# Kernel optimization log

Measured on AMD Instinct MI355X. Metric: run time of the kernel, lower is better.

Reference implementation:

```python
import jax, jax.numpy as jnp
import numpy as np

B, S, D, H, HD = 1, 4096, 1024, 16, 64
BLOCK = 128   # Fixed1/Fixed2 block_size (paper default for EnWik8)
C = 32        # Fixed2 'c' parameter
NEG = -1e10   # large negative bias for masked positions (flax make_attention_mask)


def build_sparse_mask(n: int) -> jnp.ndarray:
    """Merged Fixed1 + Fixed2 causal mask, shape [1,1,n,n] bool."""
    r = jnp.arange(n)
    q = r[:, None]
    k = r[None, :]
    lower = k <= q
    fixed1 = (q // BLOCK) == (k // BLOCK)
    rem = k % BLOCK
    fixed2 = (rem == 0) | (rem >= BLOCK - C)
    mask = lower & (fixed1 | fixed2)
    return mask[None, None, :, :]


def setup_inputs() -> dict:
    key = jax.random.key(0)
    ks = jax.random.split(key, 5)
    sc = 1.0 / np.sqrt(D)
    return {
        "x": jax.random.normal(ks[0], (B, S, D), jnp.float32),
        "Wq": jax.random.normal(ks[1], (D, H, HD), jnp.float32) * sc,
        "bq": jnp.zeros((H, HD), jnp.float32),
        "Wk": jax.random.normal(ks[2], (D, H, HD), jnp.float32) * sc,
        "bk": jnp.zeros((H, HD), jnp.float32),
        "Wv": jax.random.normal(ks[3], (D, H, HD), jnp.float32) * sc,
        "bv": jnp.zeros((H, HD), jnp.float32),
        "Wo": jax.random.normal(ks[4], (H, HD, D), jnp.float32) * (1.0 / np.sqrt(H * HD)),
        "bo": jnp.zeros((D,), jnp.float32),
    }


def reference(x, Wq, bq, Wk, bk, Wv, bv, Wo, bo):
    # QKV projections: [B,S,D] -> [B,S,H,HD]
    q = jnp.einsum("bsd,dhk->bshk", x, Wq) + bq
    k = jnp.einsum("bsd,dhk->bshk", x, Wk) + bk
    v = jnp.einsum("bsd,dhk->bshk", x, Wv) + bv

    bias = jnp.where(build_sparse_mask(S), 0.0, NEG).astype(x.dtype)

    # flax dot_product_attention: scale query, scores + bias, softmax, weighted sum
    q = q / jnp.sqrt(jnp.asarray(HD, x.dtype))
    scores = jnp.einsum("bqhd,bkhd->bhqk", q, k) + bias
    probs = jax.nn.softmax(scores, axis=-1)
    ctx = jnp.einsum("bhqk,bkhd->bqhd", probs, v)

    # output projection over (h, d) axes
    return jnp.einsum("bqhd,hdf->bqf", ctx, Wo) + bo
```

## Files before the change

### kernel.cpp

```cpp
#include <hip/hip_runtime.h>
#include <stdint.h>


#define S_LEN 4096
#define DMODEL 1024

typedef __bf16 bf16x8 __attribute__((ext_vector_type(8)));
typedef float  f32x4  __attribute__((ext_vector_type(4)));

__device__ __forceinline__ uint16_t f2bf(float f) {
    uint32_t u = __builtin_bit_cast(uint32_t, f);
    u += 0x7fffu + ((u >> 16) & 1u);
    return (uint16_t)(u >> 16);
}

__device__ __forceinline__ uint32_t pack2bf(float lo, float hi) {
    return (uint32_t)f2bf(lo) | ((uint32_t)f2bf(hi) << 16);
}

__device__ __forceinline__ void gload_lds16(const uint16_t* g, uint16_t* l) {
    __builtin_amdgcn_global_load_lds(
        (const __attribute__((address_space(1))) void*)g,
        (__attribute__((address_space(3))) void*)l, 16, 0, 0);
}

__device__ __forceinline__ int key_of(int b, int ngc, int ch, int kl) {
    if (ch >= ngc) return b * 128 + (ch - ngc) * 64 + kl;
    int t = ch * 64 + kl;
    int kb = t / 33, rr = t - kb * 33;
    return kb * 128 + (rr == 0 ? 0 : 95 + rr);
}

__global__ __launch_bounds__(256) void cvt_x_kernel(const float* __restrict__ x,
                                                    uint16_t* __restrict__ xb) {
    int i = (blockIdx.x * 256 + threadIdx.x) * 4;
    const float4 v = *(const float4*)(x + i);
    ushort4 o;
    o.x = f2bf(v.x); o.y = f2bf(v.y); o.z = f2bf(v.z); o.w = f2bf(v.w);
    *(ushort4*)(xb + i) = o;
}

__global__ __launch_bounds__(256) void tpose4(const float* __restrict__ Wq,
                                              const float* __restrict__ Wk,
                                              const float* __restrict__ Wv,
                                              const float* __restrict__ Wo,
                                              uint16_t* __restrict__ wqkvt,
                                              uint16_t* __restrict__ wot) {
    __shared__ float tile[64][65];
    const int z = blockIdx.z;
    const float* src = (z == 0) ? Wq : (z == 1) ? Wk : (z == 2) ? Wv : Wo;
    uint16_t* dst = (z < 3) ? (wqkvt + (size_t)z * 1024 * 1024) : wot;
    const int ro = blockIdx.y * 64, co = blockIdx.x * 64;
    const int c = threadIdx.x & 63, r4 = threadIdx.x >> 6;
#pragma unroll
    for (int i = 0; i < 16; i++) {
        int r = i * 4 + r4;
        tile[r][c] = src[(size_t)(ro + r) * 1024 + co + c];
    }
    __syncthreads();
#pragma unroll
    for (int i = 0; i < 16; i++) {
        int cc = i * 4 + r4;
        dst[(size_t)(co + cc) * 1024 + ro + c] = f2bf(tile[c][cc]);
    }
}

template <int MODE>
__global__ __launch_bounds__(256) void gemm_bt(const uint16_t* __restrict__ A,
                                               const uint16_t* __restrict__ Bt,
                                               const float* __restrict__ bias0,
                                               const float* __restrict__ bias1,
                                               const float* __restrict__ bias2,
                                               uint16_t* __restrict__ Cb,
                                               float* __restrict__ Cf) {
    __shared__ __attribute__((aligned(16))) uint16_t As[128 * 64];
    __shared__ __attribute__((aligned(16))) uint16_t Bs[128 * 64];
    const int tid = threadIdx.x;
    const int wave = tid >> 6, lane = tid & 63;
    const int quad = lane >> 4, l16 = lane & 15;
    const int row0 = blockIdx.y * 128, col0 = blockIdx.x * 128;
    const int wm = (wave >> 1) * 64, wn = (wave & 1) * 64;
    const int srow = lane >> 3, scol = lane & 7;
    const int gcol = (scol ^ srow) * 8;
    const int sw = (l16 & 7);

    f32x4 acc[4][4];
    const f32x4 z4 = {0.f, 0.f, 0.f, 0.f};
#pragma unroll
    for (int i = 0; i < 4; i++)
#pragma unroll
        for (int j = 0; j < 4; j++) acc[i][j] = z4;

    for (int k0 = 0; k0 < 1024; k0 += 64) {
        __syncthreads();
#pragma unroll
        for (int i = 0; i < 4; i++) {
            int u = wave * 4 + i;
            int row = u * 8 + srow;
            gload_lds16(A  + (size_t)(row0 + row) * 1024 + k0 + gcol, As + u * 512);
            gload_lds16(Bt + (size_t)(col0 + row) * 1024 + k0 + gcol, Bs + u * 512);
        }
        __syncthreads();
#pragma unroll
        for (int kk = 0; kk < 2; kk++) {
            bf16x8 af[4], bfr[4];
#pragma unroll
            for (int mt = 0; mt < 4; mt++)
                af[mt] = *(const bf16x8*)(As + (wm + mt * 16 + l16) * 64 + ((kk * 4 + quad) ^ sw) * 8);
#pragma unroll
            for (int nt = 0; nt < 4; nt++)
                bfr[nt] = *(const bf16x8*)(Bs + (wn + nt * 16 + l16) * 64 + ((kk * 4 + quad) ^ sw) * 8);
#pragma unroll
            for (int mt = 0; mt < 4; mt++)
#pragma unroll
                for (int nt = 0; nt < 4; nt++) {
                    if (MODE == 0)
                        acc[mt][nt] = __builtin_amdgcn_mfma_f32_16x16x32_bf16(
                            bfr[nt], af[mt], acc[mt][nt], 0, 0, 0);
                    else
                        acc[mt][nt] = __builtin_amdgcn_mfma_f32_16x16x32_bf16(
                            af[mt], bfr[nt], acc[mt][nt], 0, 0, 0);
                }
        }
    }

    if (MODE == 0) {
#pragma unroll
        for (int nt = 0; nt < 4; nt++) {
            int n = col0 + wn + nt * 16 + quad * 4;
            int which = n >> 10, c = n & 1023;
            const float* bp = (which == 0) ? bias0 : (which == 1 ? bias1 : bias2);
            const float4 b4 = *(const float4*)(bp + c);
            float scv = (which == 0) ? 0.125f : 1.0f;
            uint16_t* op = Cb + (size_t)which * S_LEN * 1024 + c;
#pragma unroll
            for (int mt = 0; mt < 4; mt++) {
                int s = row0 + wm + mt * 16 + l16;
                ushort4 pkv;
                pkv.x = f2bf((acc[mt][nt][0] + b4.x) * scv);
                pkv.y = f2bf((acc[mt][nt][1] + b4.y) * scv);
                pkv.z = f2bf((acc[mt][nt][2] + b4.z) * scv);
                pkv.w = f2bf((acc[mt][nt][3] + b4.w) * scv);
                *(ushort4*)(op + (size_t)s * 1024) = pkv;
            }
        }
    } else {
#pragma unroll
        for (int nt = 0; nt < 4; nt++) {
            int n = col0 + wn + nt * 16 + l16;
            float bi = bias0[n];
#pragma unroll
            for (int mt = 0; mt < 4; mt++) {
                int row = row0 + wm + mt * 16 + quad * 4;
#pragma unroll
                for (int r = 0; r < 4; r++)
                    Cf[(size_t)(row + r) * 1024 + n] = acc[mt][nt][r] + bi;
            }
        }
    }
}

__global__ __launch_bounds__(512, 4) void attn_kernel(const uint16_t* __restrict__ Qg,
                                                      const uint16_t* __restrict__ Kg,
                                                      const uint16_t* __restrict__ Vg,
                                                      uint16_t* __restrict__ Og) {
    __shared__ __attribute__((aligned(16))) uint16_t SM[32768];
    uint16_t* Qs    = SM;
    uint16_t* Kbufs = SM + 8192;
    uint16_t* Vbufs = SM + 24576;

    const int h = blockIdx.y;
    const int b = (h < 8) ? (int)blockIdx.x : (31 - (int)blockIdx.x);
    const int tid = threadIdx.x;
    const int wave = tid >> 6, lane = tid & 63;
    const int quad = lane >> 4, l16 = lane & 15;
    const int grp = wave >> 2, wq = wave & 3;
    const int sw = (l16 & 7);

    const int nprev = 33 * b;
    const int ngc = (nprev + 63) >> 6;
    const int ntot = ngc + 2;
    const int nit = (ntot + 1) >> 1;
    const size_t hoff = (size_t)h * 64;

    const int kRow = wave * 8 + (lane >> 3);
    const int gCol = ((lane & 7) ^ (lane >> 3)) * 8;

#pragma unroll
    for (int i = 0; i < 2; i++) {
        int seg = i * 8 + wave;
        int row = seg * 8 + (lane >> 3);
        gload_lds16(Qg + (size_t)(b * 128 + row) * 1024 + hoff + gCol, Qs + seg * 512);
    }
#pragma unroll
    for (int g = 0; g < 2; g++) {
        if (g < ntot) {
            int key = key_of(b, ngc, g, kRow);
            gload_lds16(Kg + (size_t)key * 1024 + hoff + gCol,
                        Kbufs + g * 4096 + wave * 512);
        }
    }
    __syncthreads();

    float m_run[2], l_run[2];
    f32x4 o[4][2];
    const f32x4 z4 = {0.f, 0.f, 0.f, 0.f};
#pragma unroll
    for (int qt = 0; qt < 2; qt++) { m_run[qt] = -3e38f; l_run[qt] = 0.f; }
#pragma unroll
    for (int mt = 0; mt < 4; mt++) { o[mt][0] = z4; o[mt][1] = z4; }

    int cur = 0;
    for (int it = 0; it < nit; it++) {
        uint4 vreg[2];
#pragma unroll
        for (int g = 0; g < 2; g++) {
            int ch = 2 * it + g;
            if (ch < ntot) {
                int key = key_of(b, ngc, ch, lane);
                vreg[g] = *(const uint4*)(Vg + (size_t)key * 1024 + hoff + wave * 8);
            }
        }
#pragma unroll
        for (int g = 0; g < 2; g++) {
            int ch = 2 * (it + 1) + g;
            if (ch < ntot) {
                int key = key_of(b, ngc, ch, kRow);
                gload_lds16(Kg + (size_t)key * 1024 + hoff + gCol,
                            Kbufs + (cur ^ 1) * 8192 + g * 4096 + wave * 512);
            }
        }

        const int myc = 2 * it + grp;
        const bool have = (myc < ntot);
        uint32_t pk[4][2][2];
        float al[2] = {1.f, 1.f};
        if (have) {
            const uint16_t* Kc = Kbufs + cur * 8192 + grp * 4096;
            f32x4 s[4][2];
#pragma unroll
            for (int kt = 0; kt < 4; kt++) { s[kt][0] = z4; s[kt][1] = z4; }
#pragma unroll
            for (int kk = 0; kk < 2; kk++) {
                bf16x8 ka[4], qb[2];
#pragma unroll
                for (int kt = 0; kt < 4; kt++)
                    ka[kt] = *(const bf16x8*)(Kc + (kt * 16 + l16) * 64 + ((kk * 4 + quad) ^ sw) * 8);
#pragma unroll
                for (int qt = 0; qt < 2; qt++)
                    qb[qt] = *(const bf16x8*)(Qs + (wq * 32 + qt * 16 + l16) * 64 + ((kk * 4 + quad) ^ sw) * 8);
#pragma unroll
                for (int kt = 0; kt < 4; kt++)
#pragma unroll
                    for (int qt = 0; qt < 2; qt++)
                        s[kt][qt] = __builtin_amdgcn_mfma_f32_16x16x32_bf16(
                            ka[kt], qb[qt], s[kt][qt], 0, 0, 0);
            }
            if (myc >= ngc) {
                int cb = myc - ngc;
#pragma unroll
                for (int kt = 0; kt < 4; kt++) {
                    int keyl = cb * 64 + kt * 16 + quad * 4;
#pragma unroll
                    for (int qt = 0; qt < 2; qt++) {
                        int ql = wq * 32 + qt * 16 + l16;
#pragma unroll
                        for (int r = 0; r < 4; r++)
                            if (keyl + r > ql) s[kt][qt][r] = -1e30f;
                    }
                }
            } else if (myc == ngc - 1) {
#pragma unroll
                for (int kt = 0; kt < 4; kt++) {
                    int tg = myc * 64 + kt * 16 + quad * 4;
#pragma unroll
                    for (int r = 0; r < 4; r++)
                        if (tg + r >= nprev) {
                            s[kt][0][r] = -1e30f;
                            s[kt][1][r] = -1e30f;
                        }
                }
            }
#pragma unroll
            for (int qt = 0; qt < 2; qt++) {
                float mx = -3e38f;
#pragma unroll
                for (int kt = 0; kt < 4; kt++)
#pragma unroll
                    for (int r = 0; r < 4; r++) mx = fmaxf(mx, s[kt][qt][r]);
                mx = fmaxf(mx, __shfl_xor(mx, 16));
                mx = fmaxf(mx, __shfl_xor(mx, 32));
                float mn = fmaxf(m_run[qt], mx);
                float sub = fmaxf(mn, -1e20f);
                al[qt] = __expf(m_run[qt] - sub);
                m_run[qt] = mn;
                float ps = 0.f;
#pragma unroll
                for (int kt = 0; kt < 4; kt++) {
                    float p0 = __expf(s[kt][qt][0] - sub);
                    float p1 = __expf(s[kt][qt][1] - sub);
                    float p2 = __expf(s[kt][qt][2] - sub);
                    float p3 = __expf(s[kt][qt][3] - sub);
                    ps += (p0 + p1) + (p2 + p3);
                    pk[kt][qt][0] = pack2bf(p0, p1);
                    pk[kt][qt][1] = pack2bf(p2, p3);
                }
                ps += __shfl_xor(ps, 16);
                ps += __shfl_xor(ps, 32);
                l_run[qt] = l_run[qt] * al[qt] + ps;
            }
        }

#pragma unroll
        for (int g = 0; g < 2; g++) {
            int ch = 2 * it + g;
            if (ch < ntot) {
                uint16_t* Vd = Vbufs + g * 4096;
                uint32_t ww[4] = {vreg[g].x, vreg[g].y, vreg[g].z, vreg[g].w};
                const int kc = (lane >> 3), kin = (lane & 7);
#pragma unroll
                for (int j = 0; j < 4; j++) {
                    int hd0 = wave * 8 + 2 * j, hd1 = hd0 + 1;
                    Vd[hd0 * 64 + ((kc ^ (hd0 & 7)) * 8 + kin)] = (uint16_t)(ww[j] & 0xffffu);
                    Vd[hd1 * 64 + ((kc ^ (hd1 & 7)) * 8 + kin)] = (uint16_t)(ww[j] >> 16);
                }
            }
        }
        __syncthreads();

        if (have) {
            const uint16_t* Vc = Vbufs + grp * 4096;
#pragma unroll
            for (int mt = 0; mt < 4; mt++)
#pragma unroll
                for (int qt = 0; qt < 2; qt++)
#pragma unroll
                    for (int r = 0; r < 4; r++) o[mt][qt][r] *= al[qt];
            const int srcA = l16 + 32 * (quad & 1);
            const bool hi = (quad >> 1) != 0;
#pragma unroll
            for (int kk = 0; kk < 2; kk++) {
                bf16x8 va[4];
#pragma unroll
                for (int mt = 0; mt < 4; mt++)
                    va[mt] = *(const bf16x8*)(Vc + (mt * 16 + l16) * 64 + ((kk * 4 + quad) ^ sw) * 8);
#pragma unroll
                for (int qt = 0; qt < 2; qt++) {
                    uint32_t u0a = (uint32_t)__shfl((int)pk[2 * kk][qt][0], srcA);
                    uint32_t u0b = (uint32_t)__shfl((int)pk[2 * kk + 1][qt][0], srcA);
                    uint32_t u1a = (uint32_t)__shfl((int)pk[2 * kk][qt][1], srcA);
                    uint32_t u1b = (uint32_t)__shfl((int)pk[2 * kk + 1][qt][1], srcA);
                    uint32_t u2a = (uint32_t)__shfl((int)pk[2 * kk][qt][0], srcA + 16);
                    uint32_t u2b = (uint32_t)__shfl((int)pk[2 * kk + 1][qt][0], srcA + 16);
                    uint32_t u3a = (uint32_t)__shfl((int)pk[2 * kk][qt][1], srcA + 16);
                    uint32_t u3b = (uint32_t)__shfl((int)pk[2 * kk + 1][qt][1], srcA + 16);
                    uint4 fr;
                    fr.x = hi ? u0b : u0a;
                    fr.y = hi ? u1b : u1a;
                    fr.z = hi ? u2b : u2a;
                    fr.w = hi ? u3b : u3a;
                    bf16x8 pb = __builtin_bit_cast(bf16x8, fr);
#pragma unroll
                    for (int mt = 0; mt < 4; mt++)
                        o[mt][qt] = __builtin_amdgcn_mfma_f32_16x16x32_bf16(
                            va[mt], pb, o[mt][qt], 0, 0, 0);
                }
            }
        }
        __syncthreads();
        cur ^= 1;
    }

    float* Obuf = (float*)(SM + 8192);
    float* mB = Obuf + 128 * 68;
    float* lB = mB + 128;
    if (grp == 1) {
#pragma unroll
        for (int qt = 0; qt < 2; qt++) {
            int ql = wq * 32 + qt * 16 + l16;
            if (quad == 0) { mB[ql] = m_run[qt]; lB[ql] = l_run[qt]; }
#pragma unroll
            for (int mt = 0; mt < 4; mt++)
                *(f32x4*)(Obuf + ql * 68 + mt * 16 + quad * 4) = o[mt][qt];
        }
    }
    __syncthreads();
    if (grp == 0) {
#pragma unroll
        for (int qt = 0; qt < 2; qt++) {
            int ql = wq * 32 + qt * 16 + l16;
            float mb = mB[ql], lb = lB[ql];
            float ms = fmaxf(m_run[qt], mb);
            float fa = __expf(m_run[qt] - ms);
            float fb = __expf(mb - ms);
            float inv = 1.0f / (l_run[qt] * fa + lb * fb);
            int q = b * 128 + ql;
#pragma unroll
            for (int mt = 0; mt < 4; mt++) {
                f32x4 ob = *(const f32x4*)(Obuf + ql * 68 + mt * 16 + quad * 4);
                ushort4 pko;
                pko.x = f2bf((o[mt][qt][0] * fa + ob[0] * fb) * inv);
                pko.y = f2bf((o[mt][qt][1] * fa + ob[1] * fb) * inv);
                pko.z = f2bf((o[mt][qt][2] * fa + ob[2] * fb) * inv);
                pko.w = f2bf((o[mt][qt][3] * fa + ob[3] * fb) * inv);
                *(ushort4*)(Og + (size_t)q * 1024 + hoff + mt * 16 + quad * 4) = pko;
            }
        }
    }
}

extern "C" void kernel_launch(void* const* d_in, const int* in_sizes, int n_in,
                              void* d_out, int out_size, void* d_ws, size_t ws_size,
                              hipStream_t stream) {
    const float* x  = (const float*)d_in[0];
    const float* Wq = (const float*)d_in[1];
    const float* bq = (const float*)d_in[2];
    const float* Wk = (const float*)d_in[3];
    const float* bk = (const float*)d_in[4];
    const float* Wv = (const float*)d_in[5];
    const float* bv = (const float*)d_in[6];
    const float* Wo = (const float*)d_in[7];
    const float* bo = (const float*)d_in[8];
    float* out = (float*)d_out;

    uint8_t* ws = (uint8_t*)d_ws;
    uint16_t* x_bf  = (uint16_t*)(ws);
    uint16_t* wqkvt = (uint16_t*)(ws + (8u << 20));
    uint16_t* wot   = (uint16_t*)(ws + (14u << 20));
    uint16_t* q_bf  = (uint16_t*)(ws + (16u << 20));
    uint16_t* k_bf  = (uint16_t*)(ws + (24u << 20));
    uint16_t* v_bf  = (uint16_t*)(ws + (32u << 20));
    uint16_t* ctx   = (uint16_t*)(ws + (40u << 20));
    if (ws_size < (48u << 20)) return;

    cvt_x_kernel<<<4096, 256, 0, stream>>>(x, x_bf);
    tpose4<<<dim3(16, 16, 4), 256, 0, stream>>>(Wq, Wk, Wv, Wo, wqkvt, wot);
    gemm_bt<0><<<dim3(24, 32), 256, 0, stream>>>(x_bf, wqkvt, bq, bk, bv,
                                                 q_bf, nullptr);
    attn_kernel<<<dim3(32, 16), 512, 0, stream>>>(q_bf, k_bf, v_bf, ctx);
    gemm_bt<1><<<dim3(8, 32), 256, 0, stream>>>(ctx, wot, bo, nullptr, nullptr,
                                                nullptr, out);
}
```

Measured before the change: 196.9 us.

## Split long attention blocks across two workgroups with a separate merge kernel

```diff
diff --git a/kernel.cpp b/kernel.cpp
--- a/kernel.cpp
+++ b/kernel.cpp
@@ -3,7 +3,6 @@
 
 
 #define S_LEN 4096
-#define DMODEL 1024
 
 typedef __bf16 bf16x8 __attribute__((ext_vector_type(8)));
 typedef float  f32x4  __attribute__((ext_vector_type(4)));
@@ -13,11 +12,13 @@
     u += 0x7fffu + ((u >> 16) & 1u);
     return (uint16_t)(u >> 16);
 }
-
+__device__ __forceinline__ float bf2f(uint16_t v) {
+    uint32_t u = (uint32_t)v << 16;
+    return __builtin_bit_cast(float, u);
+}
 __device__ __forceinline__ uint32_t pack2bf(float lo, float hi) {
     return (uint32_t)f2bf(lo) | ((uint32_t)f2bf(hi) << 16);
 }
-
 __device__ __forceinline__ void gload_lds16(const uint16_t* g, uint16_t* l) {
     __builtin_amdgcn_global_load_lds(
         (const __attribute__((address_space(1))) void*)g,
@@ -131,7 +132,7 @@
             int which = n >> 10, c = n & 1023;
             const float* bp = (which == 0) ? bias0 : (which == 1 ? bias1 : bias2);
             const float4 b4 = *(const float4*)(bp + c);
-            float scv = (which == 0) ? 0.125f : 1.0f;
+            float scv = (which == 0) ? 0.18033688f : 1.0f;
             uint16_t* op = Cb + (size_t)which * S_LEN * 1024 + c;
 #pragma unroll
             for (int mt = 0; mt < 4; mt++) {
@@ -160,252 +161,277 @@
     }
 }
 
-__global__ __launch_bounds__(512, 4) void attn_kernel(const uint16_t* __restrict__ Qg,
+__global__ __launch_bounds__(256, 4) void attn_kernel(const uint16_t* __restrict__ Qg,
                                                       const uint16_t* __restrict__ Kg,
                                                       const uint16_t* __restrict__ Vg,
-                                                      uint16_t* __restrict__ Og) {
-    __shared__ __attribute__((aligned(16))) uint16_t SM[32768];
-    uint16_t* Qs    = SM;
-    uint16_t* Kbufs = SM + 8192;
-    uint16_t* Vbufs = SM + 24576;
+                                                      uint16_t* __restrict__ Og,
+                                                      uint16_t* __restrict__ pO,
+                                                      float2* __restrict__ pStats) {
+    __shared__ __attribute__((aligned(16))) uint16_t SM[20480];
+    uint16_t* Kb = SM;
+    uint16_t* Vt = SM + 8192;
+    uint16_t* Pb = SM + 12288;
 
     const int h = blockIdx.y;
-    const int b = (h < 8) ? (int)blockIdx.x : (31 - (int)blockIdx.x);
+    const int bjob = blockIdx.x;
+    int b, slot;
+    if (bjob < 8) { b = bjob; slot = -1; }
+    else { int idx = bjob - 8; b = 8 + (idx >> 1); slot = idx * 16 + h; }
+    const int nprev = 33 * b;
+    const int ngc = (nprev + 63) >> 6;
+    const int ntot = ngc + 2;
+    int cbeg = 0, cend = ntot;
+    if (bjob >= 8) {
+        int mid = (ntot + 1) >> 1;
+        if ((bjob - 8) & 1) cbeg = mid; else cend = mid;
+    }
+    const size_t hoff = (size_t)h * 64;
+
     const int tid = threadIdx.x;
     const int wave = tid >> 6, lane = tid & 63;
     const int quad = lane >> 4, l16 = lane & 15;
-    const int grp = wave >> 2, wq = wave & 3;
-    const int sw = (l16 & 7);
-
-    const int nprev = 33 * b;
-    const int ngc = (nprev + 63) >> 6;
-    const int ntot = ngc + 2;
-    const int nit = (ntot + 1) >> 1;
-    const size_t hoff = (size_t)h * 64;
-
-    const int kRow = wave * 8 + (lane >> 3);
-    const int gCol = ((lane & 7) ^ (lane >> 3)) * 8;
+    const int sw = l16 & 7;
+    const int gCol = ((lane & 7) ^ ((lane >> 3) & 7)) * 8;
+    const int kp = tid & 31, hseg = tid >> 5;
+
+    bf16x8 qb[2][2];
+#pragma unroll
+    for (int kk = 0; kk < 2; kk++)
+#pragma unroll
+        for (int qt = 0; qt < 2; qt++) {
+            uint4 t = *(const uint4*)(Qg + (size_t)(b * 128 + wave * 32 + qt * 16 + l16) * 1024
+                                      + hoff + kk * 32 + quad * 8);
+            qb[kk][qt] = __builtin_bit_cast(bf16x8, t);
+        }
 
 #pragma unroll
     for (int i = 0; i < 2; i++) {
-        int seg = i * 8 + wave;
-        int row = seg * 8 + (lane >> 3);
-        gload_lds16(Qg + (size_t)(b * 128 + row) * 1024 + hoff + gCol, Qs + seg * 512);
-    }
-#pragma unroll
-    for (int g = 0; g < 2; g++) {
-        if (g < ntot) {
-            int key = key_of(b, ngc, g, kRow);
-            gload_lds16(Kg + (size_t)key * 1024 + hoff + gCol,
-                        Kbufs + g * 4096 + wave * 512);
-        }
+        int u = wave * 2 + i;
+        int row = u * 8 + (lane >> 3);
+        int key = key_of(b, ngc, cbeg, row);
+        gload_lds16(Kg + (size_t)key * 1024 + hoff + gCol, Kb + u * 512);
     }
     __syncthreads();
 
-    float m_run[2], l_run[2];
+    float m_run[2] = {-3e38f, -3e38f}, l_run[2] = {0.f, 0.f};
     f32x4 o[4][2];
     const f32x4 z4 = {0.f, 0.f, 0.f, 0.f};
 #pragma unroll
-    for (int qt = 0; qt < 2; qt++) { m_run[qt] = -3e38f; l_run[qt] = 0.f; }
-#pragma unroll
     for (int mt = 0; mt < 4; mt++) { o[mt][0] = z4; o[mt][1] = z4; }
 
+    uint16_t* Pw = Pb + wave * 2048;
     int cur = 0;
-    for (int it = 0; it < nit; it++) {
-        uint4 vreg[2];
-#pragma unroll
-        for (int g = 0; g < 2; g++) {
-            int ch = 2 * it + g;
-            if (ch < ntot) {
-                int key = key_of(b, ngc, ch, lane);
-                vreg[g] = *(const uint4*)(Vg + (size_t)key * 1024 + hoff + wave * 8);
-            }
-        }
-#pragma unroll
-        for (int g = 0; g < 2; g++) {
-            int ch = 2 * (it + 1) + g;
-            if (ch < ntot) {
-                int key = key_of(b, ngc, ch, kRow);
+
+    for (int ci = cbeg; ci < cend; ci++) {
+        int vk0 = key_of(b, ngc, ci, 2 * kp);
+        int vk1 = key_of(b, ngc, ci, 2 * kp + 1);
+        uint4 va4 = *(const uint4*)(Vg + (size_t)vk0 * 1024 + hoff + hseg * 8);
+        uint4 vc4 = *(const uint4*)(Vg + (size_t)vk1 * 1024 + hoff + hseg * 8);
+
+        if (ci + 1 < cend) {
+#pragma unroll
+            for (int i = 0; i < 2; i++) {
+                int u = wave * 2 + i;
+                int row = u * 8 + (lane >> 3);
+                int key = key_of(b, ngc, ci + 1, row);
                 gload_lds16(Kg + (size_t)key * 1024 + hoff + gCol,
-                            Kbufs + (cur ^ 1) * 8192 + g * 4096 + wave * 512);
-            }
-        }
-
-        const int myc = 2 * it + grp;
-        const bool have = (myc < ntot);
+                            Kb + (cur ^ 1) * 4096 + u * 512);
+            }
+        }
+
+        const uint16_t* Kc = Kb + cur * 4096;
+        f32x4 s[4][2];
+#pragma unroll
+        for (int kt = 0; kt < 4; kt++) { s[kt][0] = z4; s[kt][1] = z4; }
+#pragma unroll
+        for (int kk = 0; kk < 2; kk++) {
+            bf16x8 ka[4];
+#pragma unroll
+            for (int kt = 0; kt < 4; kt++)
+                ka[kt] = *(const bf16x8*)(Kc + (kt * 16 + l16) * 64 + ((kk * 4 + quad) ^ sw) * 8);
+#pragma unroll
+            for (int kt = 0; kt < 4; kt++)
+#pragma unroll
+                for (int qt = 0; qt < 2; qt++)
+                    s[kt][qt] = __builtin_amdgcn_mfma_f32_16x16x32_bf16(
+                        ka[kt], qb[kk][qt], s[kt][qt], 0, 0, 0);
+        }
+
+        if (ci >= ngc) {
+            int cb = ci - ngc;
+#pragma unroll
+            for (int kt = 0; kt < 4; kt++) {
+                int keyl = cb * 64 + kt * 16 + quad * 4;
+#pragma unroll
+                for (int qt = 0; qt < 2; qt++) {
+                    int ql = wave * 32 + qt * 16 + l16;
+#pragma unroll
+                    for (int r = 0; r < 4; r++)
+                        if (keyl + r > ql) s[kt][qt][r] = -1e30f;
+                }
+            }
+        } else if (ci == ngc - 1) {
+#pragma unroll
+            for (int kt = 0; kt < 4; kt++) {
+                int tg = ci * 64 + kt * 16 + quad * 4;
+#pragma unroll
+                for (int r = 0; r < 4; r++)
+                    if (tg + r >= nprev) { s[kt][0][r] = -1e30f; s[kt][1][r] = -1e30f; }
+            }
+        }
+
         uint32_t pk[4][2][2];
-        float al[2] = {1.f, 1.f};
-        if (have) {
-            const uint16_t* Kc = Kbufs + cur * 8192 + grp * 4096;
-            f32x4 s[4][2];
-#pragma unroll
-            for (int kt = 0; kt < 4; kt++) { s[kt][0] = z4; s[kt][1] = z4; }
-#pragma unroll
-            for (int kk = 0; kk < 2; kk++) {
-                bf16x8 ka[4], qb[2];
-#pragma unroll
-                for (int kt = 0; kt < 4; kt++)
-                    ka[kt] = *(const bf16x8*)(Kc + (kt * 16 + l16) * 64 + ((kk * 4 + quad) ^ sw) * 8);
+        float al[2];
+#pragma unroll
+        for (int qt = 0; qt < 2; qt++) {
+            float mx = -3e38f;
+#pragma unroll
+            for (int kt = 0; kt < 4; kt++)
+#pragma unroll
+                for (int r = 0; r < 4; r++) mx = fmaxf(mx, s[kt][qt][r]);
+            mx = fmaxf(mx, __shfl_xor(mx, 16));
+            mx = fmaxf(mx, __shfl_xor(mx, 32));
+            float mn = fmaxf(m_run[qt], mx);
+            float sub = fmaxf(mn, -1e20f);
+            al[qt] = exp2f(m_run[qt] - sub);
+            m_run[qt] = mn;
+            float ps = 0.f;
+#pragma unroll
+            for (int kt = 0; kt < 4; kt++) {
+                float p0 = exp2f(s[kt][qt][0] - sub);
+                float p1 = exp2f(s[kt][qt][1] - sub);
+                float p2 = exp2f(s[kt][qt][2] - sub);
+                float p3 = exp2f(s[kt][qt][3] - sub);
+                ps += (p0 + p1) + (p2 + p3);
+                pk[kt][qt][0] = pack2bf(p0, p1);
+                pk[kt][qt][1] = pack2bf(p2, p3);
+            }
+            ps += __shfl_xor(ps, 16);
+            ps += __shfl_xor(ps, 32);
+            l_run[qt] = l_run[qt] * al[qt] + ps;
+        }
+
+#pragma unroll
+        for (int qt = 0; qt < 2; qt++) {
+            int row = qt * 16 + l16;
+            int rs = row & 7;
+#pragma unroll
+            for (int kt = 0; kt < 4; kt++) {
+                int g = kt * 2 + (quad >> 1);
+                uint2 val = make_uint2(pk[kt][qt][0], pk[kt][qt][1]);
+                *(uint2*)(Pw + row * 64 + ((g ^ rs) * 8) + (quad & 1) * 4) = val;
+            }
+        }
+
+        __syncthreads();
+
+        {
+            uint32_t av[4] = {va4.x, va4.y, va4.z, va4.w};
+            uint32_t cv[4] = {vc4.x, vc4.y, vc4.z, vc4.w};
+#pragma unroll
+            for (int j = 0; j < 4; j++) {
+                uint32_t lo = (av[j] & 0xffffu) | (cv[j] << 16);
+                uint32_t hi = (av[j] >> 16) | (cv[j] & 0xffff0000u);
+                int hd0 = hseg * 8 + 2 * j, hd1 = hd0 + 1;
+                *(uint32_t*)(Vt + hd0 * 64 + (((kp >> 2) ^ (hd0 & 7)) * 8) + (kp & 3) * 2) = lo;
+                *(uint32_t*)(Vt + hd1 * 64 + (((kp >> 2) ^ (hd1 & 7)) * 8) + (kp & 3) * 2) = hi;
+            }
+        }
+
+        __syncthreads();
+
+#pragma unroll
+        for (int mt = 0; mt < 4; mt++)
+#pragma unroll
+            for (int qt = 0; qt < 2; qt++)
+#pragma unroll
+                for (int r = 0; r < 4; r++) o[mt][qt][r] *= al[qt];
+#pragma unroll
+        for (int kk = 0; kk < 2; kk++) {
+            bf16x8 vaf[4], pbf[2];
+#pragma unroll
+            for (int mt = 0; mt < 4; mt++)
+                vaf[mt] = *(const bf16x8*)(Vt + (mt * 16 + l16) * 64 + ((kk * 4 + quad) ^ sw) * 8);
+#pragma unroll
+            for (int qt = 0; qt < 2; qt++) {
+                int row = qt * 16 + l16;
+                pbf[qt] = *(const bf16x8*)(Pw + row * 64 + (((kk * 4 + quad) ^ (row & 7)) * 8));
+            }
+#pragma unroll
+            for (int mt = 0; mt < 4; mt++)
 #pragma unroll
                 for (int qt = 0; qt < 2; qt++)
-                    qb[qt] = *(const bf16x8*)(Qs + (wq * 32 + qt * 16 + l16) * 64 + ((kk * 4 + quad) ^ sw) * 8);
-#pragma unroll
-                for (int kt = 0; kt < 4; kt++)
-#pragma unroll
-                    for (int qt = 0; qt < 2; qt++)
-                        s[kt][qt] = __builtin_amdgcn_mfma_f32_16x16x32_bf16(
-                            ka[kt], qb[qt], s[kt][qt], 0, 0, 0);
-            }
-            if (myc >= ngc) {
-                int cb = myc - ngc;
-#pragma unroll
-                for (int kt = 0; kt < 4; kt++) {
-                    int keyl = cb * 64 + kt * 16 + quad * 4;
-#pragma unroll
-                    for (int qt = 0; qt < 2; qt++) {
-                        int ql = wq * 32 + qt * 16 + l16;
-#pragma unroll
-                        for (int r = 0; r < 4; r++)
-                            if (keyl + r > ql) s[kt][qt][r] = -1e30f;
-                    }
-                }
-            } else if (myc == ngc - 1) {
-#pragma unroll
-                for (int kt = 0; kt < 4; kt++) {
-                    int tg = myc * 64 + kt * 16 + quad * 4;
-#pragma unroll
-                    for (int r = 0; r < 4; r++)
-                        if (tg + r >= nprev) {
-                            s[kt][0][r] = -1e30f;
-                            s[kt][1][r] = -1e30f;
-                        }
-                }
-            }
-#pragma unroll
-            for (int qt = 0; qt < 2; qt++) {
-                float mx = -3e38f;
-#pragma unroll
-                for (int kt = 0; kt < 4; kt++)
-#pragma unroll
-                    for (int r = 0; r < 4; r++) mx = fmaxf(mx, s[kt][qt][r]);
-                mx = fmaxf(mx, __shfl_xor(mx, 16));
-                mx = fmaxf(mx, __shfl_xor(mx, 32));
-                float mn = fmaxf(m_run[qt], mx);
-                float sub = fmaxf(mn, -1e20f);
-                al[qt] = __expf(m_run[qt] - sub);
-                m_run[qt] = mn;
-                float ps = 0.f;
-#pragma unroll
-                for (int kt = 0; kt < 4; kt++) {
-                    float p0 = __expf(s[kt][qt][0] - sub);
-                    float p1 = __expf(s[kt][qt][1] - sub);
-                    float p2 = __expf(s[kt][qt][2] - sub);
-                    float p3 = __expf(s[kt][qt][3] - sub);
-                    ps += (p0 + p1) + (p2 + p3);
-                    pk[kt][qt][0] = pack2bf(p0, p1);
-                    pk[kt][qt][1] = pack2bf(p2, p3);
-                }
-                ps += __shfl_xor(ps, 16);
-                ps += __shfl_xor(ps, 32);
-                l_run[qt] = l_run[qt] * al[qt] + ps;
-            }
-        }
-
-#pragma unroll
-        for (int g = 0; g < 2; g++) {
-            int ch = 2 * it + g;
-            if (ch < ntot) {
-                uint16_t* Vd = Vbufs + g * 4096;
-                uint32_t ww[4] = {vreg[g].x, vreg[g].y, vreg[g].z, vreg[g].w};
-                const int kc = (lane >> 3), kin = (lane & 7);
-#pragma unroll
-                for (int j = 0; j < 4; j++) {
-                    int hd0 = wave * 8 + 2 * j, hd1 = hd0 + 1;
-                    Vd[hd0 * 64 + ((kc ^ (hd0 & 7)) * 8 + kin)] = (uint16_t)(ww[j] & 0xffffu);
-                    Vd[hd1 * 64 + ((kc ^ (hd1 & 7)) * 8 + kin)] = (uint16_t)(ww[j] >> 16);
-                }
-            }
-        }
-        __syncthreads();
-
-        if (have) {
-            const uint16_t* Vc = Vbufs + grp * 4096;
-#pragma unroll
-            for (int mt = 0; mt < 4; mt++)
-#pragma unroll
-                for (int qt = 0; qt < 2; qt++)
-#pragma unroll
-                    for (int r = 0; r < 4; r++) o[mt][qt][r] *= al[qt];
-            const int srcA = l16 + 32 * (quad & 1);
-            const bool hi = (quad >> 1) != 0;
-#pragma unroll
-            for (int kk = 0; kk < 2; kk++) {
-                bf16x8 va[4];
-#pragma unroll
-                for (int mt = 0; mt < 4; mt++)
-                    va[mt] = *(const bf16x8*)(Vc + (mt * 16 + l16) * 64 + ((kk * 4 + quad) ^ sw) * 8);
-#pragma unroll
-                for (int qt = 0; qt < 2; qt++) {
-                    uint32_t u0a = (uint32_t)__shfl((int)pk[2 * kk][qt][0], srcA);
-                    uint32_t u0b = (uint32_t)__shfl((int)pk[2 * kk + 1][qt][0], srcA);
-                    uint32_t u1a = (uint32_t)__shfl((int)pk[2 * kk][qt][1], srcA);
-                    uint32_t u1b = (uint32_t)__shfl((int)pk[2 * kk + 1][qt][1], srcA);
-                    uint32_t u2a = (uint32_t)__shfl((int)pk[2 * kk][qt][0], srcA + 16);
-                    uint32_t u2b = (uint32_t)__shfl((int)pk[2 * kk + 1][qt][0], srcA + 16);
-                    uint32_t u3a = (uint32_t)__shfl((int)pk[2 * kk][qt][1], srcA + 16);
-                    uint32_t u3b = (uint32_t)__shfl((int)pk[2 * kk + 1][qt][1], srcA + 16);
-                    uint4 fr;
-                    fr.x = hi ? u0b : u0a;
-                    fr.y = hi ? u1b : u1a;
-                    fr.z = hi ? u2b : u2a;
-                    fr.w = hi ? u3b : u3a;
-                    bf16x8 pb = __builtin_bit_cast(bf16x8, fr);
-#pragma unroll
-                    for (int mt = 0; mt < 4; mt++)
-                        o[mt][qt] = __builtin_amdgcn_mfma_f32_16x16x32_bf16(
-                            va[mt], pb, o[mt][qt], 0, 0, 0);
-                }
-            }
+                    o[mt][qt] = __builtin_amdgcn_mfma_f32_16x16x32_bf16(
+                        vaf[mt], pbf[qt], o[mt][qt], 0, 0, 0);
         }
         __syncthreads();
         cur ^= 1;
     }
 
-    float* Obuf = (float*)(SM + 8192);
-    float* mB = Obuf + 128 * 68;
-    float* lB = mB + 128;
-    if (grp == 1) {
+    if (slot < 0) {
 #pragma unroll
         for (int qt = 0; qt < 2; qt++) {
-            int ql = wq * 32 + qt * 16 + l16;
-            if (quad == 0) { mB[ql] = m_run[qt]; lB[ql] = l_run[qt]; }
-#pragma unroll
-            for (int mt = 0; mt < 4; mt++)
-                *(f32x4*)(Obuf + ql * 68 + mt * 16 + quad * 4) = o[mt][qt];
-        }
-    }
-    __syncthreads();
-    if (grp == 0) {
+            float inv = 1.0f / l_run[qt];
+            int q = b * 128 + wave * 32 + qt * 16 + l16;
+#pragma unroll
+            for (int mt = 0; mt < 4; mt++) {
+                ushort4 pko;
+                pko.x = f2bf(o[mt][qt][0] * inv);
+                pko.y = f2bf(o[mt][qt][1] * inv);
+                pko.z = f2bf(o[mt][qt][2] * inv);
+                pko.w = f2bf(o[mt][qt][3] * inv);
+                *(ushort4*)(Og + (size_t)q * 1024 + hoff + mt * 16 + quad * 4) = pko;
+            }
+        }
+    } else {
+        uint16_t* po = pO + (size_t)slot * 8192;
 #pragma unroll
         for (int qt = 0; qt < 2; qt++) {
-            int ql = wq * 32 + qt * 16 + l16;
-            float mb = mB[ql], lb = lB[ql];
-            float ms = fmaxf(m_run[qt], mb);
-            float fa = __expf(m_run[qt] - ms);
-            float fb = __expf(mb - ms);
-            float inv = 1.0f / (l_run[qt] * fa + lb * fb);
-            int q = b * 128 + ql;
+            int q = wave * 32 + qt * 16 + l16;
+            if (quad == 0) pStats[slot * 128 + q] = make_float2(m_run[qt], l_run[qt]);
 #pragma unroll
             for (int mt = 0; mt < 4; mt++) {
-                f32x4 ob = *(const f32x4*)(Obuf + ql * 68 + mt * 16 + quad * 4);
                 ushort4 pko;
-                pko.x = f2bf((o[mt][qt][0] * fa + ob[0] * fb) * inv);
-                pko.y = f2bf((o[mt][qt][1] * fa + ob[1] * fb) * inv);
-                pko.z = f2bf((o[mt][qt][2] * fa + ob[2] * fb) * inv);
-                pko.w = f2bf((o[mt][qt][3] * fa + ob[3] * fb) * inv);
-                *(ushort4*)(Og + (size_t)q * 1024 + hoff + mt * 16 + quad * 4) = pko;
-            }
-        }
+                pko.x = f2bf(o[mt][qt][0]);
+                pko.y = f2bf(o[mt][qt][1]);
+                pko.z = f2bf(o[mt][qt][2]);
+                pko.w = f2bf(o[mt][qt][3]);
+                *(ushort4*)(po + q * 64 + mt * 16 + quad * 4) = pko;
+            }
+        }
+    }
+}
+
+__global__ __launch_bounds__(256) void attn_merge(const uint16_t* __restrict__ pO,
+                                                  const float2* __restrict__ pStats,
+                                                  uint16_t* __restrict__ Og) {
+    const int b = 8 + blockIdx.x, h = blockIdx.y;
+    const int tid = threadIdx.x;
+    const int q = tid >> 1, hh = tid & 1;
+    const int s0 = ((b - 8) * 2) * 16 + h, s1 = s0 + 16;
+    float2 st0 = pStats[s0 * 128 + q];
+    float2 st1 = pStats[s1 * 128 + q];
+    float m = fmaxf(st0.x, st1.x);
+    float f0 = exp2f(st0.x - m), f1 = exp2f(st1.x - m);
+    float inv = 1.0f / (st0.y * f0 + st1.y * f1);
+    f0 *= inv; f1 *= inv;
+    const uint16_t* p0 = pO + (size_t)s0 * 8192 + q * 64 + hh * 32;
+    const uint16_t* p1 = pO + (size_t)s1 * 8192 + q * 64 + hh * 32;
+    uint16_t* od = Og + (size_t)(b * 128 + q) * 1024 + h * 64 + hh * 32;
+#pragma unroll
+    for (int i = 0; i < 4; i++) {
+        uint4 a = *(const uint4*)(p0 + i * 8);
+        uint4 c = *(const uint4*)(p1 + i * 8);
+        uint32_t av[4] = {a.x, a.y, a.z, a.w}, cv[4] = {c.x, c.y, c.z, c.w};
+        uint32_t ov[4];
+#pragma unroll
+        for (int j = 0; j < 4; j++) {
+            float r0 = bf2f((uint16_t)(av[j] & 0xffffu)) * f0 + bf2f((uint16_t)(cv[j] & 0xffffu)) * f1;
+            float r1 = bf2f((uint16_t)(av[j] >> 16)) * f0 + bf2f((uint16_t)(cv[j] >> 16)) * f1;
+            ov[j] = pack2bf(r0, r1);
+        }
+        uint4 w = {ov[0], ov[1], ov[2], ov[3]};
+        *(uint4*)(od + i * 8) = w;
     }
 }
 
@@ -431,13 +457,16 @@
     uint16_t* k_bf  = (uint16_t*)(ws + (24u << 20));
     uint16_t* v_bf  = (uint16_t*)(ws + (32u << 20));
     uint16_t* ctx   = (uint16_t*)(ws + (40u << 20));
+    uint16_t* pO    = (uint16_t*)(ws);
+    float2*   pSt   = (float2*)(ws + (13u << 20));
     if (ws_size < (48u << 20)) return;
 
     cvt_x_kernel<<<4096, 256, 0, stream>>>(x, x_bf);
     tpose4<<<dim3(16, 16, 4), 256, 0, stream>>>(Wq, Wk, Wv, Wo, wqkvt, wot);
     gemm_bt<0><<<dim3(24, 32), 256, 0, stream>>>(x_bf, wqkvt, bq, bk, bv,
                                                  q_bf, nullptr);
-    attn_kernel<<<dim3(32, 16), 512, 0, stream>>>(q_bf, k_bf, v_bf, ctx);
+    attn_kernel<<<dim3(56, 16), 256, 0, stream>>>(q_bf, k_bf, v_bf, ctx, pO, pSt);
+    attn_merge<<<dim3(24, 16), 256, 0, stream>>>(pO, pSt, ctx);
     gemm_bt<1><<<dim3(8, 32), 256, 0, stream>>>(ctx, wot, bo, nullptr, nullptr,
                                                 nullptr, out);
 }
```

Result: slower. 237.0 us (+20.4%).
